# Optimization experiments

Measured on AMD Instinct MI355X. Metric: run time of the kernel, lower is better.

The kernel has to match this reference:

```python
import jax, jax.numpy as jnp
import numpy as np

SMOOTH = 1e-5  # MONAI DiceLoss smooth_nr / smooth_dr defaults
BETA = 1.0


def setup_inputs() -> dict:
    key = jax.random.key(0)
    k1, k2, k3 = jax.random.split(key, 3)
    B, C, H, W = 8, 16, 512, 512
    outputs = jax.random.normal(k1, (B, C, H, W), dtype=jnp.float32)
    targets = jax.random.randint(k2, (B, 1, H, W), 0, C, dtype=jnp.int64)
    matrix_penalty = jax.random.uniform(k3, (C, C), dtype=jnp.float32)
    return {
        "outputs": outputs,
        "targets": targets,
        "matrix_penalty": matrix_penalty,
        "N_classes": C,
        "Npixels": H * W,
        "length_targets": B,
        "total_batch": B,
    }


def _domino_loss(outputs, matrix_penalty, t, N_classes, total_batch):
    # outputs: [B, C, H, W] logits; t: [B, H, W] int labels
    logp = jax.nn.log_softmax(outputs, axis=1)          # [B, C, H, W]
    probs = jnp.exp(logp)
    probs_bhwc = jnp.moveaxis(probs, 1, -1)             # [B, H, W, C]
    onehot = jax.nn.one_hot(t, N_classes, dtype=outputs.dtype)  # [B, H, W, C]

    # Cross-entropy term (mean over all pixels), as in CrossEntropyLoss
    ce = -jnp.mean(jnp.sum(onehot * jnp.moveaxis(logp, 1, -1), axis=-1))

    # Dice term (softmax probs vs one-hot target, per batch x class, mean)
    inter = jnp.sum(probs_bhwc * onehot, axis=(1, 2))   # [B, C]
    denom = jnp.sum(probs_bhwc, axis=(1, 2)) + jnp.sum(onehot, axis=(1, 2))
    dice = jnp.mean(1.0 - (2.0 * inter + SMOOTH) / (denom + SMOOTH))

    # DOMINO penalty: per pixel, one_hot(target)^T @ matrix_penalty @ softmax(logits)
    # = matrix_penalty[target] . probs  (gather row instead of tiny matmul)
    pen_rows = matrix_penalty[t]                        # [B, H, W, C]
    penalty = jnp.sum(pen_rows * probs_bhwc)

    return ce + dice + BETA * penalty / total_batch


def reference(outputs, targets, matrix_penalty, N_classes, Npixels, length_targets, total_batch):
    t = targets[:, 0].astype(jnp.int32)                 # [B, H, W]
    return _domino_loss(outputs, matrix_penalty, t, N_classes, total_batch)
```

## Files before the change

kernel.cpp:

```cpp
#include <hip/hip_runtime.h>

#define NC      16
#define HW      (512 * 512)
#define NB      8
#define BPB     32
#define NBLK    (NB * BPB)
#define THREADS 1024
#define PXR     1024
#define ROUNDS  8
#define SMOOTH  1e-5f

__global__ __launch_bounds__(THREADS) void domino_main(
    const float* __restrict__ logits,
    const int*   __restrict__ tgt,
    const float* __restrict__ penalty,
    float*       __restrict__ P)
{
    __shared__ float bufA[NC * PXR];
    __shared__ float bufB[NC * PXR];
    __shared__ float pen_t[NC * NC];
    __shared__ float red[16][34];

    const int tid  = threadIdx.x;
    const int w    = tid >> 6;
    const int lane = tid & 63;
    const int b    = blockIdx.x / BPB;
    const int blk  = blockIdx.x % BPB;

    if (tid < NC * NC) {
        const int r = tid / NC, c = tid % NC;
        pen_t[c * NC + r] = penalty[tid];
    }

    const float* ob   = logits + (size_t)b * NC * HW;
    const int*   tb   = tgt    + (size_t)b * HW;
    const float* cls  = ob + (size_t)w * HW;
    const int    base = blk * (ROUNDS * PXR);

    {
        const float4 a0 = *(const float4*)(cls + base +   0 + lane * 4);
        const float4 a1 = *(const float4*)(cls + base + 256 + lane * 4);
        const float4 a2 = *(const float4*)(cls + base + 512 + lane * 4);
        const float4 a3 = *(const float4*)(cls + base + 768 + lane * 4);
        *(float4*)&bufA[w * PXR +   0 + lane * 4] = a0;
        *(float4*)&bufA[w * PXR + 256 + lane * 4] = a1;
        *(float4*)&bufA[w * PXR + 512 + lane * 4] = a2;
        *(float4*)&bufA[w * PXR + 768 + lane * 4] = a3;
    }
    int tcur = tb[base + tid];

    float inter_acc[NC], denom_acc[NC];
#pragma unroll
    for (int c = 0; c < NC; ++c) { inter_acc[c] = 0.f; denom_acc[c] = 0.f; }
    float ce_acc = 0.f, pen_acc = 0.f;

    __syncthreads();

    for (int r = 0; r < ROUNDS; ++r) {
        float* const curb = (r & 1) ? bufB : bufA;
        float* const nxtb = (r & 1) ? bufA : bufB;

        float4 g0, g1, g2, g3;
        int tn = 0;
        if (r + 1 < ROUNDS) {
            const int p1 = base + (r + 1) * PXR;
            g0 = *(const float4*)(cls + p1 +   0 + lane * 4);
            g1 = *(const float4*)(cls + p1 + 256 + lane * 4);
            g2 = *(const float4*)(cls + p1 + 512 + lane * 4);
            g3 = *(const float4*)(cls + p1 + 768 + lane * 4);
            tn = tb[p1 + tid];
        }

        {
            const int t = tcur;
            float e[NC], s = 0.f;
#pragma unroll
            for (int c = 0; c < NC; ++c) {
                e[c] = __expf(curb[c * PXR + tid]);
                s += e[c];
            }
            float et = 0.f;
#pragma unroll
            for (int c = 0; c < NC; ++c) et = (t == c) ? e[c] : et;
            const float inv = 1.0f / s;
            ce_acc -= __logf(et * inv);
            float pdot = 0.f;
#pragma unroll
            for (int c = 0; c < NC; ++c) {
                const float p = e[c] * inv;
                denom_acc[c] += p + ((t == c) ? 1.f : 0.f);
                inter_acc[c] += (t == c) ? p : 0.f;
                pdot += pen_t[c * NC + t] * p;
            }
            pen_acc += pdot;
        }

        if (r + 1 < ROUNDS) {
            *(float4*)&nxtb[w * PXR +   0 + lane * 4] = g0;
            *(float4*)&nxtb[w * PXR + 256 + lane * 4] = g1;
            *(float4*)&nxtb[w * PXR + 512 + lane * 4] = g2;
            *(float4*)&nxtb[w * PXR + 768 + lane * 4] = g3;
            tcur = tn;
        }
        __syncthreads();
    }

#pragma unroll
    for (int c = 0; c < NC; ++c) {
#pragma unroll
        for (int off = 32; off; off >>= 1) {
            inter_acc[c] += __shfl_xor(inter_acc[c], off);
            denom_acc[c] += __shfl_xor(denom_acc[c], off);
        }
    }
#pragma unroll
    for (int off = 32; off; off >>= 1) {
        ce_acc  += __shfl_xor(ce_acc,  off);
        pen_acc += __shfl_xor(pen_acc, off);
    }

    if (lane == 0) {
#pragma unroll
        for (int c = 0; c < NC; ++c) {
            red[w][c]      = inter_acc[c];
            red[w][NC + c] = denom_acc[c];
        }
        red[w][32] = ce_acc;
        red[w][33] = pen_acc;
    }
    __syncthreads();

    if (tid < 34) {
        float v = 0.f;
#pragma unroll
        for (int i = 0; i < 16; ++i) v += red[i][tid];
        P[tid * NBLK + blockIdx.x] = v;
    }
}

__global__ __launch_bounds__(256) void domino_final(
    const float* __restrict__ P, float* __restrict__ out)
{
    __shared__ float dice_l[128], ce_l[4], pen_l[4], dice_w[2];

    const int tid = threadIdx.x;
    const int bin = tid >> 1, j = tid & 1;
    const int c = bin >> 3, bb = bin & 7;

    const float* ip = P + (size_t)c        * NBLK + bb * BPB + j * 16;
    const float* dp = P + (size_t)(NC + c) * NBLK + bb * BPB + j * 16;
    float inter = 0.f, denom = 0.f;
#pragma unroll
    for (int k = 0; k < 4; ++k) {
        const float4 a = *(const float4*)(ip + 4 * k); inter += a.x + a.y + a.z + a.w;
        const float4 d = *(const float4*)(dp + 4 * k); denom += d.x + d.y + d.z + d.w;
    }
    inter += __shfl_xor(inter, 1);
    denom += __shfl_xor(denom, 1);
    if (j == 0)
        dice_l[bin] = 1.0f - (2.0f * inter + SMOOTH) / (denom + SMOOTH);

    float ce  = P[32 * NBLK + tid];
    float pen = P[33 * NBLK + tid];
#pragma unroll
    for (int off = 32; off; off >>= 1) {
        ce  += __shfl_xor(ce,  off);
        pen += __shfl_xor(pen, off);
    }
    const int lane = tid & 63, wid = tid >> 6;
    if (lane == 0) { ce_l[wid] = ce; pen_l[wid] = pen; }
    __syncthreads();

    if (tid < 128) {
        float d = dice_l[tid];
#pragma unroll
        for (int off = 32; off; off >>= 1) d += __shfl_xor(d, off);
        if ((tid & 63) == 0) dice_w[tid >> 6] = d;
    }
    __syncthreads();

    if (tid == 0) {
        out[0] = (ce_l[0] + ce_l[1] + ce_l[2] + ce_l[3]) * (1.0f / (8.0f * 262144.0f))
               + (dice_w[0] + dice_w[1]) * (1.0f / 128.0f)
               + (pen_l[0] + pen_l[1] + pen_l[2] + pen_l[3]) * (1.0f / 8.0f);
    }
}

extern "C" void kernel_launch(void* const* d_in, const int* in_sizes, int n_in,
                              void* d_out, int out_size, void* d_ws, size_t ws_size,
                              hipStream_t stream)
{
    const float* logits = (const float*)d_in[0];
    const int*   tgt    = (const int*)d_in[1];
    const float* pen    = (const float*)d_in[2];
    float*       P      = (float*)d_ws;
    float*       out    = (float*)d_out;

    domino_main<<<NBLK, THREADS, 0, stream>>>(logits, tgt, pen, P);
    domino_final<<<1, 256, 0, stream>>>(P, out);
}
```

Baseline: 38.90 us.

## Stage logits directly to LDS via global_load_lds with smaller blocks and rotated start

Logit tiles now go straight from global memory into LDS with the async global_load_lds builtin, so they no longer pass through registers and separate LDS stores. Blocks shrink to 512 threads covering 512 pixels per round, which doubles the block count and lets each wave stage two classes. Each block also starts at a rotated round offset to spread concurrent accesses across memory channels. The final reduction kernel is adjusted to the new partial-sum count. This adds reliance on the LDS-direct load path and its synchronisation via __syncthreads.

```diff
diff --git a/kernel.cpp b/kernel.cpp
--- a/kernel.cpp
+++ b/kernel.cpp
@@ -3,14 +3,22 @@
 #define NC      16
 #define HW      (512 * 512)
 #define NB      8
-#define BPB     32
+#define BPB     64
 #define NBLK    (NB * BPB)
-#define THREADS 1024
-#define PXR     1024
+#define THREADS 512
+#define PXR     512
 #define ROUNDS  8
 #define SMOOTH  1e-5f
 
-__global__ __launch_bounds__(THREADS) void domino_main(
+typedef __attribute__((address_space(3))) unsigned int       lds_u32;
+typedef __attribute__((address_space(1))) const unsigned int glb_u32;
+
+__device__ __forceinline__ void stage16(const float* g, float* l) {
+    __builtin_amdgcn_global_load_lds((glb_u32*)(const void*)g,
+                                     (lds_u32*)(void*)l, 16, 0, 0);
+}
+
+__global__ __launch_bounds__(THREADS, 4) void domino_main(
     const float* __restrict__ logits,
     const int*   __restrict__ tgt,
     const float* __restrict__ penalty,
@@ -19,13 +27,14 @@
     __shared__ float bufA[NC * PXR];
     __shared__ float bufB[NC * PXR];
     __shared__ float pen_t[NC * NC];
-    __shared__ float red[16][34];
+    __shared__ float red[8][34];
 
     const int tid  = threadIdx.x;
     const int w    = tid >> 6;
     const int lane = tid & 63;
     const int b    = blockIdx.x / BPB;
     const int blk  = blockIdx.x % BPB;
+    const int rot  = blockIdx.x & 7;
 
     if (tid < NC * NC) {
         const int r = tid / NC, c = tid % NC;
@@ -34,20 +43,19 @@
 
     const float* ob   = logits + (size_t)b * NC * HW;
     const int*   tb   = tgt    + (size_t)b * HW;
-    const float* cls  = ob + (size_t)w * HW;
     const int    base = blk * (ROUNDS * PXR);
+    const int    c0   = 2 * w, c1 = 2 * w + 1;
+    const float* s0   = ob + (size_t)c0 * HW + base;
+    const float* s1   = ob + (size_t)c1 * HW + base;
 
     {
-        const float4 a0 = *(const float4*)(cls + base +   0 + lane * 4);
-        const float4 a1 = *(const float4*)(cls + base + 256 + lane * 4);
-        const float4 a2 = *(const float4*)(cls + base + 512 + lane * 4);
-        const float4 a3 = *(const float4*)(cls + base + 768 + lane * 4);
-        *(float4*)&bufA[w * PXR +   0 + lane * 4] = a0;
-        *(float4*)&bufA[w * PXR + 256 + lane * 4] = a1;
-        *(float4*)&bufA[w * PXR + 512 + lane * 4] = a2;
-        *(float4*)&bufA[w * PXR + 768 + lane * 4] = a3;
-    }
-    int tcur = tb[base + tid];
+        const int off = rot * PXR;
+        stage16(s0 + off +   0 + lane * 4, &bufA[c0 * PXR +   0]);
+        stage16(s0 + off + 256 + lane * 4, &bufA[c0 * PXR + 256]);
+        stage16(s1 + off +   0 + lane * 4, &bufA[c1 * PXR +   0]);
+        stage16(s1 + off + 256 + lane * 4, &bufA[c1 * PXR + 256]);
+    }
+    int tcur = tb[base + rot * PXR + tid];
 
     float inter_acc[NC], denom_acc[NC];
 #pragma unroll
@@ -60,15 +68,14 @@
         float* const curb = (r & 1) ? bufB : bufA;
         float* const nxtb = (r & 1) ? bufA : bufB;
 
-        float4 g0, g1, g2, g3;
         int tn = 0;
         if (r + 1 < ROUNDS) {
-            const int p1 = base + (r + 1) * PXR;
-            g0 = *(const float4*)(cls + p1 +   0 + lane * 4);
-            g1 = *(const float4*)(cls + p1 + 256 + lane * 4);
-            g2 = *(const float4*)(cls + p1 + 512 + lane * 4);
-            g3 = *(const float4*)(cls + p1 + 768 + lane * 4);
-            tn = tb[p1 + tid];
+            const int off = ((r + 1 + rot) & 7) * PXR;
+            stage16(s0 + off +   0 + lane * 4, &nxtb[c0 * PXR +   0]);
+            stage16(s0 + off + 256 + lane * 4, &nxtb[c0 * PXR + 256]);
+            stage16(s1 + off +   0 + lane * 4, &nxtb[c1 * PXR +   0]);
+            stage16(s1 + off + 256 + lane * 4, &nxtb[c1 * PXR + 256]);
+            tn = tb[base + off + tid];
         }
 
         {
@@ -95,14 +102,8 @@
             pen_acc += pdot;
         }
 
-        if (r + 1 < ROUNDS) {
-            *(float4*)&nxtb[w * PXR +   0 + lane * 4] = g0;
-            *(float4*)&nxtb[w * PXR + 256 + lane * 4] = g1;
-            *(float4*)&nxtb[w * PXR + 512 + lane * 4] = g2;
-            *(float4*)&nxtb[w * PXR + 768 + lane * 4] = g3;
-            tcur = tn;
-        }
         __syncthreads();
+        tcur = tn;
     }
 
 #pragma unroll
@@ -133,18 +134,18 @@
     if (tid < 34) {
         float v = 0.f;
 #pragma unroll
-        for (int i = 0; i < 16; ++i) v += red[i][tid];
+        for (int i = 0; i < 8; ++i) v += red[i][tid];
         P[tid * NBLK + blockIdx.x] = v;
     }
 }
 
-__global__ __launch_bounds__(256) void domino_final(
+__global__ __launch_bounds__(512) void domino_final(
     const float* __restrict__ P, float* __restrict__ out)
 {
-    __shared__ float dice_l[128], ce_l[4], pen_l[4], dice_w[2];
+    __shared__ float dice_l[128], ce_l[8], pen_l[8], dice_w[2];
 
     const int tid = threadIdx.x;
-    const int bin = tid >> 1, j = tid & 1;
+    const int bin = tid >> 2, j = tid & 3;
     const int c = bin >> 3, bb = bin & 7;
 
     const float* ip = P + (size_t)c        * NBLK + bb * BPB + j * 16;
@@ -155,8 +156,11 @@
         const float4 a = *(const float4*)(ip + 4 * k); inter += a.x + a.y + a.z + a.w;
         const float4 d = *(const float4*)(dp + 4 * k); denom += d.x + d.y + d.z + d.w;
     }
-    inter += __shfl_xor(inter, 1);
-    denom += __shfl_xor(denom, 1);
+#pragma unroll
+    for (int off = 2; off; off >>= 1) {
+        inter += __shfl_xor(inter, off);
+        denom += __shfl_xor(denom, off);
+    }
     if (j == 0)
         dice_l[bin] = 1.0f - (2.0f * inter + SMOOTH) / (denom + SMOOTH);
 
@@ -180,9 +184,12 @@
     __syncthreads();
 
     if (tid == 0) {
-        out[0] = (ce_l[0] + ce_l[1] + ce_l[2] + ce_l[3]) * (1.0f / (8.0f * 262144.0f))
+        float ces = 0.f, pens = 0.f;
+#pragma unroll
+        for (int i = 0; i < 8; ++i) { ces += ce_l[i]; pens += pen_l[i]; }
+        out[0] = ces * (1.0f / (8.0f * 262144.0f))
                + (dice_w[0] + dice_w[1]) * (1.0f / 128.0f)
-               + (pen_l[0] + pen_l[1] + pen_l[2] + pen_l[3]) * (1.0f / 8.0f);
+               + pens * (1.0f / 8.0f);
     }
 }
 
@@ -197,5 +204,5 @@
     float*       out    = (float*)d_out;
 
     domino_main<<<NBLK, THREADS, 0, stream>>>(logits, tgt, pen, P);
-    domino_final<<<1, 256, 0, stream>>>(P, out);
-}
+    domino_final<<<1, 512, 0, stream>>>(P, out);
+}
```

Measured after the change: 38.47 us (median of 2 runs). Within noise of the previous version (-1.1%).
